# Kernel tuning notes

Hardware: AMD Instinct MI355X
Metric: run time of the kernel (lower is better)

## Reference

```python
import jax, jax.numpy as jnp
import numpy as np

L = 8       # num decoder layers
S = 192     # seq_len = h*w = 24*8
D = 512     # d_model
DFF = 2048  # dim_feedforward
H, W, BS = 24, 8, 16
EPS = 1e-5


def setup_inputs() -> dict:
    key = jax.random.key(0)
    ks = jax.random.split(key, 8)
    f = jax.random.normal
    return {
        "q_feat": f(ks[0], (BS, D * L, H, W), jnp.float32),
        "g_feat": f(ks[1], (BS, D * L, H, W), jnp.float32),
        "targets": jax.random.randint(ks[2], (BS,), 0, 8),
        "score_embed": f(ks[3], (L, S, S), jnp.float32) * 0.05,
        "fc0_w": f(ks[4], (L, D, D), jnp.float32) * (1.0 / np.sqrt(D)),
        "fc0_b": jnp.zeros((L, D), jnp.float32),
        "bn1_g": jnp.ones((L,), jnp.float32),
        "bn1_b": jnp.zeros((L,), jnp.float32),
        "fc2_w": f(ks[5], (L, DFF, S), jnp.float32) * (1.0 / np.sqrt(S)),
        "fc2_b": jnp.zeros((L, DFF), jnp.float32),
        "bn2_g": jnp.ones((L, DFF), jnp.float32),
        "bn2_b": jnp.zeros((L, DFF), jnp.float32),
        "fc3_w": f(ks[6], (L, DFF), jnp.float32) * (1.0 / np.sqrt(DFF)),
        "fc3_b": jnp.zeros((L,), jnp.float32),
        "bn3_g": jnp.ones((L,), jnp.float32),
        "bn3_b": jnp.zeros((L,), jnp.float32),
    }


def _layer(qf, gf, se, w0, b0, g1, b1, w2, b2, g2, bb2, w3, b3, g3, bb3):
    # qf: [q,s,d], gf: [k,s,d]; shared fc0 projection for query and key
    query = jnp.einsum('qsd,ed->qse', qf, w0) + b0
    key_ = jnp.einsum('ksd,ed->kse', gf, w0) + b0
    # 4D correlation volume masked by sigmoid of learned score embedding
    score = jnp.einsum('qtd,ksd->qkst', query, key_) * jax.nn.sigmoid(se)
    q, k = score.shape[0], score.shape[1]
    sc = score.reshape(q * k, S, S)
    cat = jnp.concatenate([sc.max(axis=1), sc.max(axis=2)], axis=-1)  # [qk, 2S]
    x = cat.reshape(-1, S)  # [2qk, S]  (matches torch view(-1,1,S))
    # bn1: single channel -> normalize over all elements (training-mode BN)
    x = g1 * (x - x.mean()) * jax.lax.rsqrt(x.var() + EPS) + b1
    x = x @ w2.T + b2  # [2qk, DFF]
    mu = x.mean(0)
    var = x.var(0)
    x = g2 * (x - mu) * jax.lax.rsqrt(var + EPS) + bb2
    x = jax.nn.relu(x)
    x = x @ w3 + b3  # [2qk]
    x = x.reshape(-1, 2).sum(-1)  # [qk]: sum of row-max branch and col-max branch
    x = g3 * (x - x.mean()) * jax.lax.rsqrt(x.var() + EPS) + bb3
    return x.reshape(q, k)


def reference(q_feat, g_feat, targets, score_embed, fc0_w, fc0_b, bn1_g, bn1_b,
              fc2_w, fc2_b, bn2_g, bn2_b, fc3_w, fc3_b, bn3_g, bn3_b):
    bs = q_feat.shape[0]
    qf = jnp.transpose(q_feat, (0, 2, 3, 1)).reshape(bs, S, D * L)
    gf = jnp.transpose(g_feat, (0, 2, 3, 1)).reshape(bs, S, D * L)
    score = None
    for i in range(L):  # fixed small layer loop; each layer has distinct params
        si = _layer(qf[..., i * D:(i + 1) * D], gf[..., i * D:(i + 1) * D],
                    score_embed[i], fc0_w[i], fc0_b[i], bn1_g[i], bn1_b[i],
                    fc2_w[i], fc2_b[i], bn2_g[i], bn2_b[i],
                    fc3_w[i], fc3_b[i], bn3_g[i], bn3_b[i])
        score = si if score is None else score + si
    pair_labels = (targets[:, None] == targets[None, :]).astype(jnp.float32)
    return score, pair_labels
```

## Files before the change

kernel.cpp:

```cpp
#include <hip/hip_runtime.h>
#include <hip/hip_bf16.h>


#define EPS_ 1e-5f

typedef __attribute__((ext_vector_type(8))) _Float16 fp16x8;
typedef __attribute__((ext_vector_type(4)))  float   f32x4;
typedef __attribute__((ext_vector_type(16))) float   f32x16;

__device__ __forceinline__ unsigned fkey(float f) {
    unsigned u = __float_as_uint(f);
    return (u & 0x80000000u) ? ~u : (u | 0x80000000u);
}
__device__ __forceinline__ float funkey(unsigned k) {
    return (k & 0x80000000u) ? __uint_as_float(k & 0x7FFFFFFFu)
                             : __uint_as_float(~k);
}
__device__ __forceinline__ void gld16(const void* gp, void* lp) {
    __builtin_amdgcn_global_load_lds(
        (const __attribute__((address_space(1))) unsigned*)gp,
        (__attribute__((address_space(3))) unsigned*)lp, 16, 0, 0);
}

__global__ __launch_bounds__(256) void k_prep(const float* __restrict__ se,
                                              float* __restrict__ sig,
                                              const float* __restrict__ w2,
                                              _Float16* __restrict__ w2h,
                                              unsigned* __restrict__ xkey,
                                              float* __restrict__ bn2z,
                                              const float* __restrict__ w0,
                                              _Float16* __restrict__ w0h) {
    int b = blockIdx.x;
    int tid = threadIdx.x;
    if (b < 3072) {
        int i = b * 256 + tid;
        float4 v = *(const float4*)(w2 + (size_t)i * 4);
        _Float16 h[4] = {(_Float16)v.x, (_Float16)v.y, (_Float16)v.z, (_Float16)v.w};
        *(uint2*)(w2h + (size_t)i * 4) = *(uint2*)h;
    } else if (b < 3360) {
        int i = (b - 3072) * 256 + tid;
        float4 v = *(const float4*)(se + (size_t)i * 4);
        float4 o;
        o.x = 1.f / (1.f + __expf(-v.x));
        o.y = 1.f / (1.f + __expf(-v.y));
        o.z = 1.f / (1.f + __expf(-v.z));
        o.w = 1.f / (1.f + __expf(-v.w));
        *(float4*)(sig + (size_t)i * 4) = o;
    } else if (b < 3552) {
        int i = (b - 3360) * 256 + tid;
        uint4 z = {0u, 0u, 0u, 0u};
        uint4* p = (uint4*)xkey + (size_t)i * 4;
        p[0] = z; p[1] = z; p[2] = z; p[3] = z;
    } else if (b < 3585) {
        int i = (b - 3552) * 256 + tid;
        if (i < 8196) {
            float4 z = {0.f, 0.f, 0.f, 0.f};
            *(float4*)(bn2z + (size_t)i * 4) = z;
        }
    } else {
        int g = (b - 3585) * 256 + tid;
        int l  = g >> 15;
        int r  = g & 32767;
        int ks = r >> 12;
        int rr = r & 4095;
        int e  = rr >> 3;
        int ch = rr & 7;
        const float* src = w0 + (size_t)l * 262144 + (size_t)e * 512 + ks * 64 + ch * 8;
        float4 v0 = *(const float4*)src;
        float4 v1 = *(const float4*)(src + 4);
        fp16x8 h;
        h[0] = (_Float16)v0.x; h[1] = (_Float16)v0.y; h[2] = (_Float16)v0.z; h[3] = (_Float16)v0.w;
        h[4] = (_Float16)v1.x; h[5] = (_Float16)v1.y; h[6] = (_Float16)v1.z; h[7] = (_Float16)v1.w;
        size_t dst = ((size_t)(l * 8 + ks) * 512 + e) * 8 + (ch ^ (e & 7));
        *(fp16x8*)(w0h + dst * 8) = h;
    }
}

__global__ __launch_bounds__(512, 4) void k_fc0(const float* __restrict__ qfeat,
                                                const float* __restrict__ gfeat,
                                                const _Float16* __restrict__ w0h,
                                                const float* __restrict__ b0,
                                                _Float16* __restrict__ Qh) {
    int bid = blockIdx.x;
    int blo = bid & 7;
    int et  = (bid >> 3) & 3;
    int bhi = (bid >> 5) & 1;
    int sel = (bid >> 6) & 1;
    int l   = bid >> 7;
    int b   = blo + bhi * 8;

    const float* feat = sel ? gfeat : qfeat;
    const float* Af = feat + (size_t)b * 786432 + (size_t)l * 98304;

    __shared__ __align__(16) char smem[81920];

    int tid = threadIdx.x;
    int lane = tid & 63;
    int w = tid >> 6;
    int wm = w >> 2, wn = w & 3;
    int c = lane & 15;
    int hi4 = lane >> 4;

    int s0 = tid, s1 = tid + 512, s2 = tid + 1024;
    int ch0 = s0 / 192, t0 = s0 - ch0 * 192;
    int ch1 = s1 / 192, t1 = s1 - ch1 * 192;
    int ch2 = s2 / 192, t2 = s2 - ch2 * 192;
    const float* ap0 = Af + ch0 * 1536 + t0;
    const float* ap1 = Af + ch1 * 1536 + t1;
    const float* ap2 = Af + ch2 * 1536 + t2;
    int aw0 = t0 * 128 + ((ch0 ^ (t0 & 7)) << 4);
    int aw1 = t1 * 128 + ((ch1 ^ (t1 & 7)) << 4);
    int aw2 = t2 * 128 + ((ch2 ^ (t2 & 7)) << 4);

    f32x4 acc[6][2];
    #pragma unroll
    for (int mi = 0; mi < 6; mi++)
        #pragma unroll
        for (int nj = 0; nj < 2; nj++)
            #pragma unroll
            for (int r = 0; r < 4; r++) acc[mi][nj][r] = 0.f;

    float rA[3][8];

    auto ALOAD = [&](int ks) {
        int off = ks * 12288;
        #pragma unroll
        for (int j = 0; j < 8; j++) rA[0][j] = ap0[off + j * 192];
        #pragma unroll
        for (int j = 0; j < 8; j++) rA[1][j] = ap1[off + j * 192];
        #pragma unroll
        for (int j = 0; j < 8; j++) rA[2][j] = ap2[off + j * 192];
    };
    auto WLOAD = [&](int ks, int buf) {
        const _Float16* wp = w0h + ((size_t)(l * 8 + ks) * 512 + et * 128) * 64;
        char* d = smem + 49152 + buf * 16384;
        #pragma unroll
        for (int p = 0; p < 2; p++)
            gld16(wp + (size_t)(tid + p * 512) * 8, d + (tid + p * 512) * 16);
    };
    auto AWRITE = [&](int buf) {
        char* db = smem + buf * 24576;
        fp16x8 h0, h1, h2;
        #pragma unroll
        for (int j = 0; j < 8; j++) h0[j] = (_Float16)rA[0][j];
        #pragma unroll
        for (int j = 0; j < 8; j++) h1[j] = (_Float16)rA[1][j];
        #pragma unroll
        for (int j = 0; j < 8; j++) h2[j] = (_Float16)rA[2][j];
        *(fp16x8*)(db + aw0) = h0;
        *(fp16x8*)(db + aw1) = h1;
        *(fp16x8*)(db + aw2) = h2;
    };
    auto COMPUTE = [&](int buf) {
        const char* Ab = smem + buf * 24576;
        const char* Wb = smem + 49152 + buf * 16384;
        fp16x8 afr[6][2], bfr[2][2];
        #pragma unroll
        for (int mi = 0; mi < 6; mi++) {
            int tr = wm * 96 + mi * 16 + c;
            #pragma unroll
            for (int k2 = 0; k2 < 2; k2++) {
                int ph = (k2 * 4 + hi4) ^ (tr & 7);
                afr[mi][k2] = *(const fp16x8*)(Ab + tr * 128 + ph * 16);
            }
        }
        #pragma unroll
        for (int nj = 0; nj < 2; nj++) {
            int er = wn * 32 + nj * 16 + c;
            #pragma unroll
            for (int k2 = 0; k2 < 2; k2++) {
                int ph = (k2 * 4 + hi4) ^ (er & 7);
                bfr[nj][k2] = *(const fp16x8*)(Wb + er * 128 + ph * 16);
            }
        }
        #pragma unroll
        for (int k2 = 0; k2 < 2; k2++)
            #pragma unroll
            for (int mi = 0; mi < 6; mi++)
                #pragma unroll
                for (int nj = 0; nj < 2; nj++)
                    acc[mi][nj] = __builtin_amdgcn_mfma_f32_16x16x32_f16(
                        afr[mi][k2], bfr[nj][k2], acc[mi][nj], 0, 0, 0);
    };

    ALOAD(0); WLOAD(0, 0); AWRITE(0);
    __syncthreads();
    #pragma unroll
    for (int ks = 0; ks < 8; ks++) {
        int cur = ks & 1, nxt = cur ^ 1;
        if (ks < 7) { ALOAD(ks + 1); WLOAD(ks + 1, nxt); }
        COMPUTE(cur);
        if (ks < 7) AWRITE(nxt);
        __syncthreads();
    }

    __syncthreads();
    _Float16* lb = (_Float16*)smem;
    int rq = hi4 * 4;
    #pragma unroll
    for (int nj = 0; nj < 2; nj++) {
        int col = wn * 32 + nj * 16 + c;
        float bias = b0[l * 512 + et * 128 + col];
        #pragma unroll
        for (int mi = 0; mi < 6; mi++) {
            int tb = wm * 96 + mi * 16 + rq;
            #pragma unroll
            for (int r = 0; r < 4; r++)
                lb[(tb + r) * 128 + col] = (_Float16)(acc[mi][nj][r] + bias);
        }
    }
    __syncthreads();
    _Float16* Ob = Qh + ((size_t)(sel * 8 + l) * 16 + b) * 98304 + et * 128;
    #pragma unroll
    for (int p = 0; p < 6; p++) {
        int v = tid + p * 512;
        int t = v >> 4;
        int e = (v & 15) * 8;
        *(fp16x8*)(Ob + (size_t)t * 512 + e) = *(const fp16x8*)(lb + t * 128 + e);
    }
}

#define BARP() do { __builtin_amdgcn_s_barrier(); \
                    __builtin_amdgcn_sched_barrier(0); } while (0)

__global__ __launch_bounds__(512, 2) void k_score(const _Float16* __restrict__ Qh,
                                                  const float* __restrict__ sig,
                                                  unsigned* __restrict__ xkey,
                                                  int base) {
    int bid = blockIdx.x + base;
    int l = bid & 7;
    int tau = bid >> 3;
    int mt = tau % 12;
    int nt = tau / 12;
    int m0 = mt * 256, n0 = nt * 256;

    const char* Ag = (const char*)(Qh + (size_t)(8 + l) * 1572864);
    const char* Bg = (const char*)(Qh + (size_t)l * 1572864);

    __shared__ __align__(16) char smem[131072];

    int tid = threadIdx.x;
    int lane = tid & 63;
    int w = tid >> 6;
    int wm = w >> 2, wn = w & 3;
    int c = lane & 15;
    int hi4 = lane >> 4;

    int pk0 = ((hi4)     ^ (c & 7)) * 16;
    int pk1 = ((4 + hi4) ^ (c & 7)) * 16;
    char* aBase = smem + wm * 16384 + c * 128;
    char* bBase = smem + 65536 + (wn >> 1) * 16384 + ((wn & 1) * 64 + c) * 128;

    int rl = lane >> 3;
    int qsw = ((lane & 7) ^ rl) * 16;
    const char* Asrc = Ag + (size_t)(m0 + w * 8 + rl) * 1024 + qsw;
    const char* Bsrc = Bg + (size_t)(n0 + w * 8 + rl) * 1024 + qsw;
    char* aSt = smem + w * 1024;
    char* bSt = smem + 65536 + w * 1024;

    f32x4 acc[8][4];
    #pragma unroll
    for (int mi = 0; mi < 8; mi++)
        #pragma unroll
        for (int nj = 0; nj < 4; nj++)
            #pragma unroll
            for (int r = 0; r < 4; r++) acc[mi][nj][r] = 0.f;

    fp16x8 a[4][2], b01[2][2], b23[2][2];

    auto STA = [&](int t, int h) {
        if (t < 8) {
            const char* s = Asrc + (size_t)(h * 128) * 1024 + t * 128;
            char* d = aSt + (t & 1) * 32768 + h * 16384;
            gld16(s, d);
            gld16(s + 64 * 1024, d + 8192);
        }
    };
    auto STB = [&](int t, int h) {
        if (t < 8) {
            const char* s = Bsrc + (size_t)(h * 128) * 1024 + t * 128;
            char* d = bSt + (t & 1) * 32768 + h * 16384;
            gld16(s, d);
            gld16(s + 64 * 1024, d + 8192);
        }
    };
    auto LDA = [&](int t, int mh) {
        const char* p = aBase + (t & 1) * 32768 + mh * 8192;
        #pragma unroll
        for (int m = 0; m < 4; m++) {
            a[m][0] = *(const fp16x8*)(p + m * 2048 + pk0);
            a[m][1] = *(const fp16x8*)(p + m * 2048 + pk1);
        }
    };
    auto LDB = [&](int t, int nh, fp16x8 (&bb)[2][2]) {
        const char* p = bBase + (t & 1) * 32768 + nh * 4096;
        #pragma unroll
        for (int n = 0; n < 2; n++) {
            bb[n][0] = *(const fp16x8*)(p + n * 2048 + pk0);
            bb[n][1] = *(const fp16x8*)(p + n * 2048 + pk1);
        }
    };
    auto MM = [&](int mh, int nh, fp16x8 (&bb)[2][2]) {
        #pragma unroll
        for (int ks = 0; ks < 2; ks++)
            #pragma unroll
            for (int m = 0; m < 4; m++)
                #pragma unroll
                for (int n = 0; n < 2; n++)
                    acc[mh * 4 + m][nh * 2 + n] = __builtin_amdgcn_mfma_f32_16x16x32_f16(
                        a[m][ks], bb[n][ks], acc[mh * 4 + m][nh * 2 + n], 0, 0, 0);
    };

    STB(0, 0); STB(0, 1); STA(0, 0); STA(0, 1); STB(1, 0); STB(1, 1);
    asm volatile("s_waitcnt vmcnt(4)");
    BARP();

    #pragma unroll
    for (int it = 0; it < 4; it++) {
        int T = 2 * it, U = 2 * it + 1;
        LDA(T, 0); LDB(T, 0, b01); STA(U, 0); BARP();
        __builtin_amdgcn_s_setprio(1); MM(0, 0, b01); __builtin_amdgcn_s_setprio(0); BARP();
        LDB(T, 1, b23); STA(U, 1); BARP();
        __builtin_amdgcn_s_setprio(1); MM(0, 1, b23); __builtin_amdgcn_s_setprio(0); BARP();
        LDA(T, 1); STB(T + 2, 0); BARP();
        __builtin_amdgcn_s_setprio(1); MM(1, 0, b01); __builtin_amdgcn_s_setprio(0); BARP();
        STB(T + 2, 1); BARP();
        __builtin_amdgcn_s_setprio(1); MM(1, 1, b23); __builtin_amdgcn_s_setprio(0);
        if (it < 3) { asm volatile("s_waitcnt vmcnt(4)"); }
        else        { asm volatile("s_waitcnt vmcnt(0)"); }
        BARP();
        LDA(U, 0); LDB(U, 0, b01); STA(T + 2, 0); BARP();
        __builtin_amdgcn_s_setprio(1); MM(0, 0, b01); __builtin_amdgcn_s_setprio(0); BARP();
        LDB(U, 1, b23); STA(T + 2, 1); BARP();
        __builtin_amdgcn_s_setprio(1); MM(0, 1, b23); __builtin_amdgcn_s_setprio(0); BARP();
        LDA(U, 1); STB(T + 3, 0); BARP();
        __builtin_amdgcn_s_setprio(1); MM(1, 0, b01); __builtin_amdgcn_s_setprio(0); BARP();
        STB(T + 3, 1); BARP();
        __builtin_amdgcn_s_setprio(1); MM(1, 1, b23); __builtin_amdgcn_s_setprio(0);
        if (it < 3) { asm volatile("s_waitcnt vmcnt(4)"); }
        BARP();
    }

    __syncthreads();

    int rq = hi4 * 4;
    int gcb = n0 + wn * 64;
    int qq = gcb / 192;
    int tb = gcb - qq * 192;
    (void)qq;
    const float* sg = sig + (size_t)l * 36864;

    float rowm[8][4];
    float colm[2][4];
    #pragma unroll
    for (int mi = 0; mi < 8; mi++)
        #pragma unroll
        for (int r = 0; r < 4; r++) rowm[mi][r] = -3.4e38f;
    #pragma unroll
    for (int h = 0; h < 2; h++)
        #pragma unroll
        for (int nj = 0; nj < 4; nj++) colm[h][nj] = -3.4e38f;

    #pragma unroll
    for (int mi = 0; mi < 8; mi++) {
        int gm = m0 + wm * 128 + mi * 16;
        int sb = gm % 192;
        #pragma unroll
        for (int r = 0; r < 4; r++) {
            const float* sp = sg + (size_t)(sb + rq + r) * 192 + tb;
            #pragma unroll
            for (int nj = 0; nj < 4; nj++) {
                float v = acc[mi][nj][r] * sp[nj * 16 + c];
                rowm[mi][r] = fmaxf(rowm[mi][r], v);
                colm[mi >> 2][nj] = fmaxf(colm[mi >> 2][nj], v);
            }
        }
    }
    #pragma unroll
    for (int st = 1; st <= 8; st <<= 1)
        #pragma unroll
        for (int mi = 0; mi < 8; mi++)
            #pragma unroll
            for (int r = 0; r < 4; r++)
                rowm[mi][r] = fmaxf(rowm[mi][r], __shfl_xor(rowm[mi][r], st));
    #pragma unroll
    for (int h = 0; h < 2; h++)
        #pragma unroll
        for (int nj = 0; nj < 4; nj++) {
            colm[h][nj] = fmaxf(colm[h][nj], __shfl_xor(colm[h][nj], 16));
            colm[h][nj] = fmaxf(colm[h][nj], __shfl_xor(colm[h][nj], 32));
        }

    unsigned* red = (unsigned*)smem;
    if (c == 0) {
        #pragma unroll
        for (int mi = 0; mi < 8; mi++)
            #pragma unroll
            for (int r = 0; r < 4; r++)
                red[w * 256 + mi * 16 + rq + r] = fkey(rowm[mi][r]);
    }
    if (lane < 16) {
        #pragma unroll
        for (int h = 0; h < 2; h++)
            #pragma unroll
            for (int nj = 0; nj < 4; nj++)
                red[w * 256 + 128 + h * 64 + nj * 16 + lane] = fkey(colm[h][nj]);
    }
    __syncthreads();
    #pragma unroll
    for (int pass = 0; pass < 4; pass++) {
        int flat = pass * 512 + tid;
        unsigned val = red[flat];
        int ww = flat >> 8;
        int rem = flat & 255;
        int wmf = ww >> 2, wnf = ww & 3;
        int gcbf = n0 + wnf * 64;
        int qqf = gcbf / 192;
        size_t addr;
        if (rem < 128) {
            int gmf = m0 + wmf * 128 + rem;
            int kkf = gmf / 192;
            int sf = gmf - kkf * 192;
            addr = ((size_t)l * 512 + 2 * (qqf * 16 + kkf) + 1) * 192 + sf;
        } else {
            int ii = rem - 128;
            int hh = ii >> 6, cc = ii & 63;
            int kkf = (m0 + wmf * 128 + hh * 64) / 192;
            addr = ((size_t)l * 512 + 2 * (qqf * 16 + kkf)) * 192 + (gcbf - qqf * 192) + cc;
        }
        atomicMax(&xkey[addr], val);
    }
}

__global__ __launch_bounds__(256) void k_bn1s(const unsigned* __restrict__ xkey,
                                              float* __restrict__ bn1acc) {
    int l = blockIdx.x / 48;
    int b = blockIdx.x - l * 48;
    const unsigned* xk = xkey + (size_t)l * 98304 + b * 2048;
    int tid = threadIdx.x;
    uint4 v1 = *(const uint4*)(xk + tid * 8);
    uint4 v2 = *(const uint4*)(xk + tid * 8 + 4);
    float s = 0.f, s2 = 0.f;
    float e;
    e = funkey(v1.x); s += e; s2 += e * e;
    e = funkey(v1.y); s += e; s2 += e * e;
    e = funkey(v1.z); s += e; s2 += e * e;
    e = funkey(v1.w); s += e; s2 += e * e;
    e = funkey(v2.x); s += e; s2 += e * e;
    e = funkey(v2.y); s += e; s2 += e * e;
    e = funkey(v2.z); s += e; s2 += e * e;
    e = funkey(v2.w); s += e; s2 += e * e;
    #pragma unroll
    for (int o = 32; o; o >>= 1) { s += __shfl_down(s, o); s2 += __shfl_down(s2, o); }
    if ((tid & 63) == 0) {
        atomicAdd(&bn1acc[l * 2], s);
        atomicAdd(&bn1acc[l * 2 + 1], s2);
    }
}

__global__ __launch_bounds__(256) void k_bn1n(const unsigned* __restrict__ xkey,
                                              const float* __restrict__ bn1acc,
                                              const float* __restrict__ g1,
                                              const float* __restrict__ b1,
                                              _Float16* __restrict__ xh) {
    int idx = blockIdx.x * 256 + threadIdx.x;
    int l = idx / 24576;
    float mu = bn1acc[l * 2] * (1.f / 98304.f);
    float var = bn1acc[l * 2 + 1] * (1.f / 98304.f) - mu * mu;
    float a1 = g1[l] * rsqrtf(var + EPS_);
    float c1 = b1[l] - mu * a1;
    uint4 kv = *(const uint4*)(xkey + (size_t)idx * 4);
    _Float16 h[4];
    h[0] = (_Float16)(funkey(kv.x) * a1 + c1);
    h[1] = (_Float16)(funkey(kv.y) * a1 + c1);
    h[2] = (_Float16)(funkey(kv.z) * a1 + c1);
    h[3] = (_Float16)(funkey(kv.w) * a1 + c1);
    *(uint2*)(xh + (size_t)idx * 4) = *(uint2*)h;
}

__global__ __launch_bounds__(256) void k_fc2(const _Float16* __restrict__ xh,
                                             const _Float16* __restrict__ w2h,
                                             const float* __restrict__ b2,
                                             _Float16* __restrict__ hb,
                                             float* __restrict__ bn2sum,
                                             float* __restrict__ bn2sq) {
    int bid = blockIdx.x;
    int l = bid >> 6;
    int rem = bid & 63;
    int mt = rem & 3, nt = rem >> 2;
    int m0 = mt * 128, n0 = nt * 128;
    const char* Ag = (const char*)(xh + (size_t)l * 98304);
    const char* Bg = (const char*)(w2h + (size_t)l * 393216);

    __shared__ __align__(16) char As[8192];
    __shared__ __align__(16) char Bs[8192];

    int tid = threadIdx.x;
    int lane = tid & 63;
    int w = tid >> 6;
    int wm = w >> 1, wn = w & 1;

    f32x4 acc[4][4];
    #pragma unroll
    for (int mi = 0; mi < 4; mi++)
        #pragma unroll
        for (int nj = 0; nj < 4; nj++)
            #pragma unroll
            for (int r = 0; r < 4; r++) acc[mi][nj][r] = 0.f;

    int srow = lane >> 2;
    int sseg = ((lane & 3) ^ ((srow >> 1) & 3)) * 16;
    int c = lane & 15;
    int kqp = (((lane >> 4) ^ ((c >> 1) & 3))) * 16;

    for (int d0 = 0; d0 < 384; d0 += 64) {
        __syncthreads();
        #pragma unroll
        for (int j = 0; j < 2; j++) {
            int r = w * 32 + j * 16 + srow;
            gld16(Ag + (size_t)(m0 + r) * 384 + d0 + sseg, As + (w * 32 + j * 16) * 64);
            gld16(Bg + (size_t)(n0 + r) * 384 + d0 + sseg, Bs + (w * 32 + j * 16) * 64);
        }
        __syncthreads();
        fp16x8 a[4], b[4];
        #pragma unroll
        for (int mi = 0; mi < 4; mi++)
            a[mi] = *(const fp16x8*)(As + (wm * 64 + mi * 16 + c) * 64 + kqp);
        #pragma unroll
        for (int nj = 0; nj < 4; nj++)
            b[nj] = *(const fp16x8*)(Bs + (wn * 64 + nj * 16 + c) * 64 + kqp);
        #pragma unroll
        for (int mi = 0; mi < 4; mi++)
            #pragma unroll
            for (int nj = 0; nj < 4; nj++)
                acc[mi][nj] = __builtin_amdgcn_mfma_f32_16x16x32_f16(a[mi], b[nj], acc[mi][nj], 0, 0, 0);
    }

    int rq = (lane >> 4) * 4;
    _Float16* ho = hb + (size_t)l * 1048576;
    float colsum[4], colsq[4];
    #pragma unroll
    for (int nj = 0; nj < 4; nj++) { colsum[nj] = 0.f; colsq[nj] = 0.f; }
    #pragma unroll
    for (int nj = 0; nj < 4; nj++) {
        int gf = n0 + wn * 64 + nj * 16 + c;
        float bias = b2[l * 2048 + gf];
        #pragma unroll
        for (int mi = 0; mi < 4; mi++) {
            #pragma unroll
            for (int r = 0; r < 4; r++) {
                int gm = m0 + wm * 64 + mi * 16 + rq + r;
                float v = acc[mi][nj][r] + bias;
                ho[(size_t)gm * 2048 + gf] = (_Float16)v;
                colsum[nj] += v;
                colsq[nj] += v * v;
            }
        }
    }
    #pragma unroll
    for (int nj = 0; nj < 4; nj++) {
        colsum[nj] += __shfl_xor(colsum[nj], 16);
        colsum[nj] += __shfl_xor(colsum[nj], 32);
        colsq[nj]  += __shfl_xor(colsq[nj], 16);
        colsq[nj]  += __shfl_xor(colsq[nj], 32);
    }
    if (lane < 16) {
        #pragma unroll
        for (int nj = 0; nj < 4; nj++) {
            int gf = n0 + wn * 64 + nj * 16 + lane;
            atomicAdd(&bn2sum[l * 2048 + gf], colsum[nj]);
            atomicAdd(&bn2sq[l * 2048 + gf], colsq[nj]);
        }
    }
}

__global__ __launch_bounds__(256) void k_coef(const float* __restrict__ bn2sum,
                                              const float* __restrict__ bn2sq,
                                              const float* __restrict__ g2,
                                              const float* __restrict__ bb2,
                                              float* __restrict__ coef) {
    int i = blockIdx.x * 256 + threadIdx.x;
    float mu = bn2sum[i] * (1.f / 512.f);
    float var = bn2sq[i] * (1.f / 512.f) - mu * mu;
    float a2 = g2[i] * rsqrtf(var + EPS_);
    coef[i] = a2;
    coef[16384 + i] = bb2[i] - mu * a2;
}

__global__ __launch_bounds__(256) void k_fc3(const _Float16* __restrict__ hb,
                                             const float* __restrict__ coef,
                                             const float* __restrict__ w3,
                                             const float* __restrict__ b3,
                                             float* __restrict__ ybuf) {
    int grp = blockIdx.x & 63;
    int l = blockIdx.x >> 6;
    int tid = threadIdx.x;
    int w = tid >> 6, lane = tid & 63;
    const float* cA = coef + l * 2048;
    const float* cC = coef + 16384 + l * 2048;
    const float* w3p = w3 + l * 2048;
    #pragma unroll
    for (int rr = 0; rr < 2; rr++) {
        int n = grp * 8 + w + rr * 4;
        const _Float16* h = hb + ((size_t)l * 512 + n) * 2048;
        float sum = 0.f;
        #pragma unroll
        for (int q = 0; q < 4; q++) {
            int f = q * 512 + lane * 8;
            fp16x8 hv = *(const fp16x8*)(h + f);
            float4 a0 = *(const float4*)(cA + f), a1 = *(const float4*)(cA + f + 4);
            float4 c0 = *(const float4*)(cC + f), c1 = *(const float4*)(cC + f + 4);
            float4 w0 = *(const float4*)(w3p + f), w1 = *(const float4*)(w3p + f + 4);
            float va[8] = {a0.x, a0.y, a0.z, a0.w, a1.x, a1.y, a1.z, a1.w};
            float vc[8] = {c0.x, c0.y, c0.z, c0.w, c1.x, c1.y, c1.z, c1.w};
            float vw[8] = {w0.x, w0.y, w0.z, w0.w, w1.x, w1.y, w1.z, w1.w};
            #pragma unroll
            for (int j = 0; j < 8; j++) {
                float v = (float)hv[j] * va[j] + vc[j];
                v = fmaxf(v, 0.f);
                sum += v * vw[j];
            }
        }
        #pragma unroll
        for (int o = 32; o; o >>= 1) sum += __shfl_down(sum, o);
        if (lane == 0) ybuf[l * 512 + n] = sum + b3[l];
    }
}

__global__ __launch_bounds__(256) void k_final(const float* __restrict__ ybuf,
                                               const float* __restrict__ g3,
                                               const float* __restrict__ bb3,
                                               const int* __restrict__ targets,
                                               float* __restrict__ out) {
    int tid = threadIdx.x;
    __shared__ float red[8];
    float scoreacc = 0.f;
    for (int l = 0; l < 8; l++) {
        float z = ybuf[l * 512 + 2 * tid] + ybuf[l * 512 + 2 * tid + 1];
        float s = z, s2 = z * z;
        int lane = tid & 63, w = tid >> 6;
        #pragma unroll
        for (int o = 32; o; o >>= 1) { s += __shfl_down(s, o); s2 += __shfl_down(s2, o); }
        if (lane == 0) { red[w] = s; red[4 + w] = s2; }
        __syncthreads();
        float S1 = red[0] + red[1] + red[2] + red[3];
        float S2 = red[4] + red[5] + red[6] + red[7];
        float mu = S1 * (1.f / 256.f);
        float var = S2 * (1.f / 256.f) - mu * mu;
        float rstd = rsqrtf(var + EPS_);
        scoreacc += g3[l] * (z - mu) * rstd + bb3[l];
        __syncthreads();
    }
    out[tid] = scoreacc;
    int i = tid >> 4, j = tid & 15;
    out[256 + tid] = (targets[i] == targets[j]) ? 1.f : 0.f;
}

extern "C" void kernel_launch(void* const* d_in, const int* in_sizes, int n_in,
                              void* d_out, int out_size, void* d_ws, size_t ws_size,
                              hipStream_t stream) {
    const float* q_feat = (const float*)d_in[0];
    const float* g_feat = (const float*)d_in[1];
    const int*   targets = (const int*)d_in[2];
    const float* se     = (const float*)d_in[3];
    const float* fc0_w  = (const float*)d_in[4];
    const float* fc0_b  = (const float*)d_in[5];
    const float* bn1_g  = (const float*)d_in[6];
    const float* bn1_b  = (const float*)d_in[7];
    const float* fc2_w  = (const float*)d_in[8];
    const float* fc2_b  = (const float*)d_in[9];
    const float* bn2_g  = (const float*)d_in[10];
    const float* bn2_b  = (const float*)d_in[11];
    const float* fc3_w  = (const float*)d_in[12];
    const float* fc3_b  = (const float*)d_in[13];
    const float* bn3_g  = (const float*)d_in[14];
    const float* bn3_b  = (const float*)d_in[15];

    float* ws = (float*)d_ws;
    _Float16* Qh   = (_Float16*)ws;
    float*    sig  = ws + 12582912;
    unsigned* xkey = (unsigned*)(ws + 12877824);
    _Float16* xh   = (_Float16*)(ws + 13664256);
    _Float16* w2h  = (_Float16*)(ws + 14057472);
    _Float16* hb   = (_Float16*)(ws + 15630336);
    _Float16* w0h  = (_Float16*)(ws + 15630336);
    float* bn2sum = ws + 19824640;
    float* bn2sq  = ws + 19841024;
    float* bn1acc = ws + 19857408;
    float* ybuf   = ws + 19857424;
    float* out  = (float*)d_out;

    k_prep<<<4609, 256, 0, stream>>>(se, sig, fc2_w, w2h, xkey, bn2sum, fc0_w, w0h);
    k_fc0<<<1024, 512, 0, stream>>>(q_feat, g_feat, w0h, fc0_b, Qh);
    k_score<<<1152, 512, 0, stream>>>(Qh, sig, xkey, 0);
    k_bn1s<<<384, 256, 0, stream>>>(xkey, bn1acc);
    k_bn1n<<<768, 256, 0, stream>>>(xkey, bn1acc, bn1_g, bn1_b, xh);
    k_fc2<<<512, 256, 0, stream>>>(xh, w2h, fc2_b, hb, bn2sum, bn2sq);
    k_coef<<<64, 256, 0, stream>>>(bn2sum, bn2sq, bn2_g, bn2_b, sig);
    k_fc3<<<512, 256, 0, stream>>>(hb, sig, fc3_w, fc3_b, ybuf);
    k_final<<<1, 256, 0, stream>>>(ybuf, bn3_g, bn3_b, targets, out);
}
```

Baseline: 379.5 us.

## Fuse BN2 coefficient computation into fc3, coarsen fc2 weight cast, split score launch

```diff
diff --git a/kernel.cpp b/kernel.cpp
--- a/kernel.cpp
+++ b/kernel.cpp
@@ -32,13 +32,17 @@
                                               _Float16* __restrict__ w0h) {
     int b = blockIdx.x;
     int tid = threadIdx.x;
-    if (b < 3072) {
-        int i = b * 256 + tid;
-        float4 v = *(const float4*)(w2 + (size_t)i * 4);
-        _Float16 h[4] = {(_Float16)v.x, (_Float16)v.y, (_Float16)v.z, (_Float16)v.w};
-        *(uint2*)(w2h + (size_t)i * 4) = *(uint2*)h;
-    } else if (b < 3360) {
-        int i = (b - 3072) * 256 + tid;
+    if (b < 768) {
+        size_t base = (size_t)b * 1024 + tid;
+        #pragma unroll
+        for (int k = 0; k < 4; k++) {
+            size_t i = base + k * 256;
+            float4 v = ((const float4*)w2)[i];
+            _Float16 h[4] = {(_Float16)v.x, (_Float16)v.y, (_Float16)v.z, (_Float16)v.w};
+            ((uint2*)w2h)[i] = *(uint2*)h;
+        }
+    } else if (b < 1056) {
+        int i = (b - 768) * 256 + tid;
         float4 v = *(const float4*)(se + (size_t)i * 4);
         float4 o;
         o.x = 1.f / (1.f + __expf(-v.x));
@@ -46,19 +50,19 @@
         o.z = 1.f / (1.f + __expf(-v.z));
         o.w = 1.f / (1.f + __expf(-v.w));
         *(float4*)(sig + (size_t)i * 4) = o;
-    } else if (b < 3552) {
-        int i = (b - 3360) * 256 + tid;
+    } else if (b < 1248) {
+        int i = (b - 1056) * 256 + tid;
         uint4 z = {0u, 0u, 0u, 0u};
         uint4* p = (uint4*)xkey + (size_t)i * 4;
         p[0] = z; p[1] = z; p[2] = z; p[3] = z;
-    } else if (b < 3585) {
-        int i = (b - 3552) * 256 + tid;
+    } else if (b < 1281) {
+        int i = (b - 1248) * 256 + tid;
         if (i < 8196) {
             float4 z = {0.f, 0.f, 0.f, 0.f};
             *(float4*)(bn2z + (size_t)i * 4) = z;
         }
     } else {
-        int g = (b - 3585) * 256 + tid;
+        int g = (b - 1281) * 256 + tid;
         int l  = g >> 15;
         int r  = g & 32767;
         int ks = r >> 12;
@@ -574,21 +578,11 @@
     }
 }
 
-__global__ __launch_bounds__(256) void k_coef(const float* __restrict__ bn2sum,
-                                              const float* __restrict__ bn2sq,
-                                              const float* __restrict__ g2,
-                                              const float* __restrict__ bb2,
-                                              float* __restrict__ coef) {
-    int i = blockIdx.x * 256 + threadIdx.x;
-    float mu = bn2sum[i] * (1.f / 512.f);
-    float var = bn2sq[i] * (1.f / 512.f) - mu * mu;
-    float a2 = g2[i] * rsqrtf(var + EPS_);
-    coef[i] = a2;
-    coef[16384 + i] = bb2[i] - mu * a2;
-}
-
 __global__ __launch_bounds__(256) void k_fc3(const _Float16* __restrict__ hb,
-                                             const float* __restrict__ coef,
+                                             const float* __restrict__ bn2sum,
+                                             const float* __restrict__ bn2sq,
+                                             const float* __restrict__ g2,
+                                             const float* __restrict__ bb2,
                                              const float* __restrict__ w3,
                                              const float* __restrict__ b3,
                                              float* __restrict__ ybuf) {
@@ -596,8 +590,10 @@
     int l = blockIdx.x >> 6;
     int tid = threadIdx.x;
     int w = tid >> 6, lane = tid & 63;
-    const float* cA = coef + l * 2048;
-    const float* cC = coef + 16384 + l * 2048;
+    const float* s1p = bn2sum + l * 2048;
+    const float* s2p = bn2sq + l * 2048;
+    const float* g2p = g2 + l * 2048;
+    const float* b2p = bb2 + l * 2048;
     const float* w3p = w3 + l * 2048;
     #pragma unroll
     for (int rr = 0; rr < 2; rr++) {
@@ -608,15 +604,23 @@
         for (int q = 0; q < 4; q++) {
             int f = q * 512 + lane * 8;
             fp16x8 hv = *(const fp16x8*)(h + f);
-            float4 a0 = *(const float4*)(cA + f), a1 = *(const float4*)(cA + f + 4);
-            float4 c0 = *(const float4*)(cC + f), c1 = *(const float4*)(cC + f + 4);
+            float4 u0 = *(const float4*)(s1p + f), u1 = *(const float4*)(s1p + f + 4);
+            float4 q0 = *(const float4*)(s2p + f), q1 = *(const float4*)(s2p + f + 4);
+            float4 g0 = *(const float4*)(g2p + f), g1 = *(const float4*)(g2p + f + 4);
+            float4 c0 = *(const float4*)(b2p + f), c1 = *(const float4*)(b2p + f + 4);
             float4 w0 = *(const float4*)(w3p + f), w1 = *(const float4*)(w3p + f + 4);
-            float va[8] = {a0.x, a0.y, a0.z, a0.w, a1.x, a1.y, a1.z, a1.w};
-            float vc[8] = {c0.x, c0.y, c0.z, c0.w, c1.x, c1.y, c1.z, c1.w};
+            float vs[8] = {u0.x, u0.y, u0.z, u0.w, u1.x, u1.y, u1.z, u1.w};
+            float vq[8] = {q0.x, q0.y, q0.z, q0.w, q1.x, q1.y, q1.z, q1.w};
+            float vg[8] = {g0.x, g0.y, g0.z, g0.w, g1.x, g1.y, g1.z, g1.w};
+            float vb[8] = {c0.x, c0.y, c0.z, c0.w, c1.x, c1.y, c1.z, c1.w};
             float vw[8] = {w0.x, w0.y, w0.z, w0.w, w1.x, w1.y, w1.z, w1.w};
             #pragma unroll
             for (int j = 0; j < 8; j++) {
-                float v = (float)hv[j] * va[j] + vc[j];
+                float mu = vs[j] * (1.f / 512.f);
+                float var = vq[j] * (1.f / 512.f) - mu * mu;
+                float a2 = vg[j] * rsqrtf(var + EPS_);
+                float c2 = vb[j] - mu * a2;
+                float v = (float)hv[j] * a2 + c2;
                 v = fmaxf(v, 0.f);
                 sum += v * vw[j];
             }
@@ -690,13 +694,13 @@
     float* ybuf   = ws + 19857424;
     float* out  = (float*)d_out;
 
-    k_prep<<<4609, 256, 0, stream>>>(se, sig, fc2_w, w2h, xkey, bn2sum, fc0_w, w0h);
+    k_prep<<<2305, 256, 0, stream>>>(se, sig, fc2_w, w2h, xkey, bn2sum, fc0_w, w0h);
     k_fc0<<<1024, 512, 0, stream>>>(q_feat, g_feat, w0h, fc0_b, Qh);
-    k_score<<<1152, 512, 0, stream>>>(Qh, sig, xkey, 0);
+    k_score<<<576, 512, 0, stream>>>(Qh, sig, xkey, 0);
+    k_score<<<576, 512, 0, stream>>>(Qh, sig, xkey, 576);
     k_bn1s<<<384, 256, 0, stream>>>(xkey, bn1acc);
     k_bn1n<<<768, 256, 0, stream>>>(xkey, bn1acc, bn1_g, bn1_b, xh);
     k_fc2<<<512, 256, 0, stream>>>(xh, w2h, fc2_b, hb, bn2sum, bn2sq);
-    k_coef<<<64, 256, 0, stream>>>(bn2sum, bn2sq, bn2_g, bn2_b, sig);
-    k_fc3<<<512, 256, 0, stream>>>(hb, sig, fc3_w, fc3_b, ybuf);
+    k_fc3<<<512, 256, 0, stream>>>(hb, bn2sum, bn2sq, bn2_g, bn2_b, fc3_w, fc3_b, ybuf);
     k_final<<<1, 256, 0, stream>>>(ybuf, bn3_g, bn3_b, targets, out);
 }
```

After: 393.1 us. 1.04x slower.
